# Performance work log

Hardware: AMD Instinct MI355X
Metric: run time of the kernel (lower is better)

Reference implementation:

```python
import jax, jax.numpy as jnp
import numpy as np

N, T, ENC_H, ATT_H, DEC_H, OUT, SPK = 32, 4096, 512, 256, 512, 80, 64
ATT_RANGE = 10
KW = 31  # conv kernel width, padding 15


def softsign(x):
    return x / (1.0 + jnp.abs(x))


def setup_inputs() -> dict:
    key = jax.random.key(0)
    ks = jax.random.split(key, 20)
    lengths_enc = jax.random.randint(ks[0], (N,), 2048, T + 1)
    pos = jnp.arange(T)
    prev_attention = jax.random.uniform(ks[1], (N, T, 1), jnp.float32)
    # zero attention beyond valid length (so argmax lies within length, as in practice)
    prev_attention = prev_attention * (pos[None, :, None] < lengths_enc[:, None, None])
    s = 0.05
    inp = {
        "input_enc": jax.random.normal(ks[2], (N, T, ENC_H), jnp.float32),
        "input_dec": jax.random.normal(ks[3], (N, 1, OUT), jnp.float32),
        "prev_attention": prev_attention,
        "spkr_vec": jax.random.normal(ks[4], (N, 1, SPK), jnp.float32),
        "lengths_enc": lengths_enc,
        "speed": jax.random.uniform(ks[5], (N,), jnp.float32),
        # parameters (torch Linear: y = x @ W.T + b; we store W already transposed)
        "W_enc": jax.random.normal(ks[6], (ENC_H, ATT_H), jnp.float32) * s,
        "b_enc": jnp.zeros((ATT_H,), jnp.float32),
        "W_spkr": jax.random.normal(ks[7], (SPK, ATT_H), jnp.float32) * s,
        "conv_w": jax.random.normal(ks[8], (ATT_H, 1, KW), jnp.float32) * s,  # OIH
        "W_dec": jax.random.normal(ks[9], (DEC_H, ATT_H), jnp.float32) * s,
        "W_speed": jax.random.normal(ks[10], (1, ATT_H), jnp.float32) * s,
        "Wp1": jax.random.normal(ks[11], (OUT + SPK, 2 * DEC_H), jnp.float32) * s,
        "bp1": jnp.zeros((2 * DEC_H,), jnp.float32),
        "Wp2": jax.random.normal(ks[12], (2 * DEC_H, DEC_H), jnp.float32) * s,
        "bp2": jnp.zeros((DEC_H,), jnp.float32),
        "W_proj": jax.random.normal(ks[13], (ATT_H, 1), jnp.float32) * s,
        "b_proj": jnp.zeros((1,), jnp.float32),
    }
    return inp


def reference(input_enc, input_dec, prev_attention, spkr_vec, lengths_enc, speed,
              W_enc, b_enc, W_spkr, conv_w, W_dec, W_speed,
              Wp1, bp1, Wp2, bp2, W_proj, b_proj):
    # prenet (dropout = identity in eval mode)
    dec_in = jnp.concatenate([input_dec, spkr_vec], axis=-1)          # [N,1,OUT+SPK]
    h = jax.nn.relu(dec_in @ Wp1 + bp1)                               # [N,1,2*DEC_H]
    out_prenet = jax.nn.relu(h @ Wp2 + bp2)                           # [N,1,DEC_H]

    # biases (computed fresh, null_bias branch)
    att_bias_speed = (speed[:, None] @ W_speed)[:, None, :]           # [N,1,ATT_H]
    att_bias_enc = softsign(input_enc @ W_enc + b_enc)                # [N,T,ATT_H]
    att_bias_spkr = softsign(spkr_vec @ W_spkr)                       # [N,1,ATT_H]

    # location conv: [N,T,1] -> [N,1,T] -> conv(k=31,p=15) -> [N,ATT_H,T] -> [N,T,ATT_H]
    conv = jax.lax.conv_general_dilated(
        prev_attention.transpose(0, 2, 1), conv_w,
        window_strides=(1,), padding=[(15, 15)],
        dimension_numbers=("NCH", "OIH", "NCH"))
    in_att_prev_att = conv.transpose(0, 2, 1)                         # [N,T,ATT_H]

    in_att_dec = out_prenet @ W_dec                                   # [N,1,ATT_H]

    e = att_bias_enc + in_att_dec + att_bias_spkr + in_att_prev_att + att_bias_speed
    logit = jnp.tanh(e) @ W_proj + b_proj                             # [N,T,1]

    # windowed band mask around argmax of prev attention (no_grad in torch)
    max_idx = jnp.argmax(prev_attention[:, :, 0], axis=1)             # [N]
    lo = jnp.maximum(max_idx - (ATT_RANGE - 1), 0)
    hi = jnp.minimum(max_idx + (ATT_RANGE - 1), lengths_enc - 1)
    pos = jnp.arange(T)
    att_mask = ((pos[None, :] >= lo[:, None]) & (pos[None, :] <= hi[:, None]))
    att_mask = att_mask[:, :, None].astype(logit.dtype)               # [N,T,1]

    logit_max = jnp.max(logit, axis=1, keepdims=True)
    curr = jnp.exp(logit - logit_max) * att_mask
    denom = jnp.maximum(jnp.sum(jnp.abs(curr), axis=1, keepdims=True), 1e-12)
    return curr / denom
```

## Files before the change

### kernel.cpp

```cpp
#include <hip/hip_runtime.h>
#include <hip/hip_bf16.h>

#define NB     32
#define TLEN   4096
#define ENCH   512
#define ATTH   256
#define OUTD   80
#define SPKD   64
#define KW     31
#define ATTR   10

__global__ __launch_bounds__(1024) void fused_kernel(
    const float* __restrict__ input_enc,
    const float* __restrict__ input_dec,
    const float* __restrict__ pa,
    const float* __restrict__ spkr_vec,
    const int*   __restrict__ lengths,
    const float* __restrict__ speed,
    const float* __restrict__ W_enc,
    const float* __restrict__ b_enc,
    const float* __restrict__ W_spkr,
    const float* __restrict__ conv_w,
    const float* __restrict__ W_dec,
    const float* __restrict__ W_speed,
    const float* __restrict__ Wp1,
    const float* __restrict__ bp1,
    const float* __restrict__ Wp2,
    const float* __restrict__ bp2,
    const float* __restrict__ W_proj,
    float* __restrict__ out)
{
  const int n   = blockIdx.x;
  const int tid = threadIdx.x;

  __shared__ float s_dec[144];
  __shared__ float s_h1[1024];
  __shared__ float s_op[512];
  __shared__ __align__(16) float s_red[8 * 512];
  __shared__ float s_av[1024];
  __shared__ int   s_ai[1024];
  __shared__ float s_bias[256];
  __shared__ float s_enc[4][ENCH];
  __shared__ float s_pa[52];
  __shared__ float s_part[16];
  __shared__ float s_logits[20];
  __shared__ int   s_lo, s_hi;

  ((float4*)(out + (size_t)n * TLEN))[tid] = make_float4(0.f, 0.f, 0.f, 0.f);

  if (tid < OUTD)      s_dec[tid] = input_dec[n * OUTD + tid];
  else if (tid < 144)  s_dec[tid] = spkr_vec[n * SPKD + (tid - OUTD)];

  {
    const float* p = pa + (size_t)n * TLEN;
    float bv = -1.f; int bi = 0;
    #pragma unroll
    for (int k = 0; k < TLEN / 1024; k++) {
      int t = tid + k * 1024;
      float v = p[t];
      if (v > bv) { bv = v; bi = t; }
    }
    s_av[tid] = bv; s_ai[tid] = bi;
    __syncthreads();
    for (int s = 512; s > 0; s >>= 1) {
      if (tid < s) {
        float ov = s_av[tid + s]; int oi = s_ai[tid + s];
        float mv = s_av[tid];     int mi = s_ai[tid];
        if (ov > mv || (ov == mv && oi < mi)) { s_av[tid] = ov; s_ai[tid] = oi; }
      }
      __syncthreads();
    }
    if (tid == 0) {
      int mi = s_ai[0];
      s_lo = max(mi - (ATTR - 1), 0);
      s_hi = min(mi + (ATTR - 1), lengths[n] - 1);
    }
  }

  {
    float acc = bp1[tid];
    #pragma unroll 4
    for (int i = 0; i < 144; i++)
      acc = fmaf(s_dec[i], Wp1[i * 1024 + tid], acc);
    s_h1[tid] = fmaxf(acc, 0.f);
  }
  __syncthreads();

  if (tid < 52) {
    int idx = s_lo - (KW / 2) + tid;
    s_pa[tid] = (idx >= 0 && idx < TLEN) ? pa[(size_t)n * TLEN + idx] : 0.f;
  }

  {
    const int g = tid & 127, sl = tid >> 7;
    const int k0 = g * 4;
    float4 acc = make_float4(0.f, 0.f, 0.f, 0.f);
    for (int j = sl; j < 1024; j += 8) {
      float hv = s_h1[j];
      float4 w = *(const float4*)(Wp2 + (size_t)j * 512 + k0);
      acc.x = fmaf(hv, w.x, acc.x);
      acc.y = fmaf(hv, w.y, acc.y);
      acc.z = fmaf(hv, w.z, acc.z);
      acc.w = fmaf(hv, w.w, acc.w);
    }
    *(float4*)(s_red + sl * 512 + k0) = acc;
    __syncthreads();
    if (tid < 512) {
      float v = bp2[tid];
      #pragma unroll
      for (int s2 = 0; s2 < 8; s2++) v += s_red[s2 * 512 + tid];
      s_op[tid] = fmaxf(v, 0.f);
    }
    __syncthreads();
  }

  {
    const int c = tid & 255, sl = tid >> 8;
    float acc = 0.f;
    const int kb = sl * 128;
    #pragma unroll 4
    for (int k = kb; k < kb + 128; k++)
      acc = fmaf(s_op[k], W_dec[k * 256 + c], acc);
    s_red[sl * 256 + c] = acc;
    __syncthreads();
    if (tid < 256) {
      float b = s_red[tid] + s_red[256 + tid] + s_red[512 + tid] + s_red[768 + tid];
      float sp = 0.f;
      #pragma unroll 4
      for (int i = 0; i < 64; i++)
        sp = fmaf(s_dec[OUTD + i], W_spkr[i * 256 + tid], sp);
      sp = sp / (1.f + fabsf(sp));
      s_bias[tid] = b + sp + speed[n] * W_speed[tid];
    }
  }
  __syncthreads();

  const int lo = s_lo, hi = s_hi;
  const int q  = tid >> 8;
  const int c  = tid & 255;
  const float be = b_enc[c];
  const float wp = W_proj[c];
  const float bs = s_bias[c];

  for (int g = 0; g < 5; g++) {
    {
      int e0 = tid, e1 = tid + 1024;
      int q0 = e0 >> 9, i0 = e0 & 511;
      int q1 = e1 >> 9, i1 = e1 & 511;
      int t0 = lo + g * 4 + q0;
      int t1 = lo + g * 4 + q1;
      s_enc[q0][i0] = (t0 <= hi) ? input_enc[((size_t)n * TLEN + t0) * ENCH + i0] : 0.f;
      s_enc[q1][i1] = (t1 <= hi) ? input_enc[((size_t)n * TLEN + t1) * ENCH + i1] : 0.f;
    }
    __syncthreads();

    float a0 = 0.f, a1 = 0.f;
    #pragma unroll 8
    for (int i = 0; i < ENCH; i += 2) {
      a0 = fmaf(s_enc[q][i],     W_enc[i * 256 + c],       a0);
      a1 = fmaf(s_enc[q][i + 1], W_enc[(i + 1) * 256 + c], a1);
    }
    float a = a0 + a1;

    const int slot = g * 4 + q;
    float cv = 0.f;
    #pragma unroll
    for (int k = 0; k < KW; k++)
      cv = fmaf(s_pa[slot + k], conv_w[c * KW + k], cv);

    float ss = a + be;
    ss = ss / (1.f + fabsf(ss));
    float v = tanhf(ss + bs + cv) * wp;

    #pragma unroll
    for (int off = 32; off > 0; off >>= 1) v += __shfl_down(v, off);
    if ((tid & 63) == 0) s_part[tid >> 6] = v;
    __syncthreads();
    if (tid < 4) {
      float s = s_part[tid * 4] + s_part[tid * 4 + 1]
              + s_part[tid * 4 + 2] + s_part[tid * 4 + 3];
      int t = lo + g * 4 + tid;
      s_logits[g * 4 + tid] = (t <= hi) ? s : -__builtin_inff();
    }
    __syncthreads();
  }

  if (tid < 64) {
    float l = (tid < 20) ? s_logits[tid] : -__builtin_inff();
    float m = l;
    #pragma unroll
    for (int off = 32; off > 0; off >>= 1) m = fmaxf(m, __shfl_down(m, off));
    m = __shfl(m, 0);
    float e = __expf(l - m);
    float s = e;
    #pragma unroll
    for (int off = 32; off > 0; off >>= 1) s += __shfl_down(s, off);
    s = __shfl(s, 0);
    int t = lo + tid;
    if (tid < 20 && t <= hi)
      out[(size_t)n * TLEN + t] = e / s;
  }
}

extern "C" void kernel_launch(void* const* d_in, const int* in_sizes, int n_in,
                              void* d_out, int out_size, void* d_ws, size_t ws_size,
                              hipStream_t stream) {
  const float* input_enc = (const float*)d_in[0];
  const float* input_dec = (const float*)d_in[1];
  const float* pa        = (const float*)d_in[2];
  const float* spkr_vec  = (const float*)d_in[3];
  const int*   lengths   = (const int*)  d_in[4];
  const float* speed     = (const float*)d_in[5];
  const float* W_enc     = (const float*)d_in[6];
  const float* b_enc     = (const float*)d_in[7];
  const float* W_spkr    = (const float*)d_in[8];
  const float* conv_w    = (const float*)d_in[9];
  const float* W_dec     = (const float*)d_in[10];
  const float* W_speed   = (const float*)d_in[11];
  const float* Wp1       = (const float*)d_in[12];
  const float* bp1       = (const float*)d_in[13];
  const float* Wp2       = (const float*)d_in[14];
  const float* bp2       = (const float*)d_in[15];
  const float* W_proj    = (const float*)d_in[16];

  float* out = (float*)d_out;

  hipLaunchKernelGGL(fused_kernel, dim3(NB), dim3(1024), 0, stream,
                     input_enc, input_dec, pa, spkr_vec, lengths, speed,
                     W_enc, b_enc, W_spkr, conv_w, W_dec, W_speed,
                     Wp1, bp1, Wp2, bp2, W_proj, out);
}
```

Before: 507.5 us.

## Split fused kernel into prep, per-timestep band, and softmax kernels

Splits the single 32-block fused kernel into three launches. A prep kernel computes the argmax window and the per-batch bias into workspace. A band kernel runs a 32x20 grid, one block per windowed timestep, with a float4-vectorized W_enc GEMV and conv weights staged in shared memory. A small softmax kernel finishes the normalization. This spreads the serial band loop across many more CUs, at the cost of two extra launches and workspace round-trips.

```diff
diff --git a/kernel.cpp b/kernel.cpp
--- a/kernel.cpp
+++ b/kernel.cpp
@@ -10,25 +10,22 @@
 #define KW     31
 #define ATTR   10
 
-__global__ __launch_bounds__(1024) void fused_kernel(
-    const float* __restrict__ input_enc,
+__global__ __launch_bounds__(1024) void prep_kernel(
+    const float* __restrict__ pa,
     const float* __restrict__ input_dec,
-    const float* __restrict__ pa,
     const float* __restrict__ spkr_vec,
-    const int*   __restrict__ lengths,
     const float* __restrict__ speed,
-    const float* __restrict__ W_enc,
-    const float* __restrict__ b_enc,
-    const float* __restrict__ W_spkr,
-    const float* __restrict__ conv_w,
-    const float* __restrict__ W_dec,
-    const float* __restrict__ W_speed,
     const float* __restrict__ Wp1,
     const float* __restrict__ bp1,
     const float* __restrict__ Wp2,
     const float* __restrict__ bp2,
-    const float* __restrict__ W_proj,
-    float* __restrict__ out)
+    const float* __restrict__ W_dec,
+    const float* __restrict__ W_spkr,
+    const float* __restrict__ W_speed,
+    const int*   __restrict__ lengths,
+    float* __restrict__ out,
+    int* __restrict__ ws_idx,
+    float* __restrict__ ws_bias)
 {
   const int n   = blockIdx.x;
   const int tid = threadIdx.x;
@@ -39,12 +36,6 @@
   __shared__ __align__(16) float s_red[8 * 512];
   __shared__ float s_av[1024];
   __shared__ int   s_ai[1024];
-  __shared__ float s_bias[256];
-  __shared__ float s_enc[4][ENCH];
-  __shared__ float s_pa[52];
-  __shared__ float s_part[16];
-  __shared__ float s_logits[20];
-  __shared__ int   s_lo, s_hi;
 
   ((float4*)(out + (size_t)n * TLEN))[tid] = make_float4(0.f, 0.f, 0.f, 0.f);
 
@@ -72,8 +63,8 @@
     }
     if (tid == 0) {
       int mi = s_ai[0];
-      s_lo = max(mi - (ATTR - 1), 0);
-      s_hi = min(mi + (ATTR - 1), lengths[n] - 1);
+      ws_idx[n * 2]     = max(mi - (ATTR - 1), 0);
+      ws_idx[n * 2 + 1] = min(mi + (ATTR - 1), lengths[n] - 1);
     }
   }
 
@@ -85,11 +76,6 @@
     s_h1[tid] = fmaxf(acc, 0.f);
   }
   __syncthreads();
-
-  if (tid < 52) {
-    int idx = s_lo - (KW / 2) + tid;
-    s_pa[tid] = (idx >= 0 && idx < TLEN) ? pa[(size_t)n * TLEN + idx] : 0.f;
-  }
 
   {
     const int g = tid & 127, sl = tid >> 7;
@@ -130,76 +116,113 @@
       for (int i = 0; i < 64; i++)
         sp = fmaf(s_dec[OUTD + i], W_spkr[i * 256 + tid], sp);
       sp = sp / (1.f + fabsf(sp));
-      s_bias[tid] = b + sp + speed[n] * W_speed[tid];
-    }
-  }
-  __syncthreads();
-
-  const int lo = s_lo, hi = s_hi;
-  const int q  = tid >> 8;
-  const int c  = tid & 255;
-  const float be = b_enc[c];
-  const float wp = W_proj[c];
-  const float bs = s_bias[c];
-
-  for (int g = 0; g < 5; g++) {
-    {
-      int e0 = tid, e1 = tid + 1024;
-      int q0 = e0 >> 9, i0 = e0 & 511;
-      int q1 = e1 >> 9, i1 = e1 & 511;
-      int t0 = lo + g * 4 + q0;
-      int t1 = lo + g * 4 + q1;
-      s_enc[q0][i0] = (t0 <= hi) ? input_enc[((size_t)n * TLEN + t0) * ENCH + i0] : 0.f;
-      s_enc[q1][i1] = (t1 <= hi) ? input_enc[((size_t)n * TLEN + t1) * ENCH + i1] : 0.f;
-    }
-    __syncthreads();
-
-    float a0 = 0.f, a1 = 0.f;
+      ws_bias[n * 256 + tid] = b + sp + speed[n] * W_speed[tid];
+    }
+  }
+}
+
+__global__ __launch_bounds__(256) void band_kernel(
+    const float* __restrict__ input_enc,
+    const float* __restrict__ pa,
+    const float* __restrict__ W_enc,
+    const float* __restrict__ b_enc,
+    const float* __restrict__ conv_w,
+    const float* __restrict__ W_proj,
+    const int*   __restrict__ ws_idx,
+    const float* __restrict__ ws_bias,
+    float* __restrict__ ws_logits)
+{
+  const int n   = blockIdx.x;
+  const int j   = blockIdx.y;
+  const int tid = threadIdx.x;
+
+  const int lo = ws_idx[n * 2];
+  const int hi = ws_idx[n * 2 + 1];
+  const int t  = lo + j;
+
+  if (t > hi) {
+    if (tid == 0) ws_logits[n * 20 + j] = -__builtin_inff();
+    return;
+  }
+
+  __shared__ __align__(16) float s_enc[ENCH];
+  __shared__ float s_pa[KW];
+  __shared__ __align__(16) float s_red[4 * 256];
+  __shared__ float s_cw[ATTH * KW];
+  __shared__ float s_part[4];
+
+  for (int k2 = tid; k2 < ATTH * KW; k2 += 256) s_cw[k2] = conv_w[k2];
+  if (tid < 128)
+    ((float4*)s_enc)[tid] = ((const float4*)(input_enc + ((size_t)n * TLEN + t) * ENCH))[tid];
+  else if (tid < 128 + KW) {
+    int idx = t - (KW / 2) + (tid - 128);
+    s_pa[tid - 128] = (idx >= 0 && idx < TLEN) ? pa[(size_t)n * TLEN + idx] : 0.f;
+  }
+  __syncthreads();
+
+  {
+    const int sl = tid >> 6;
+    const int l4 = tid & 63;
+    const float4* W4 = (const float4*)W_enc;
+    float4 acc = make_float4(0.f, 0.f, 0.f, 0.f);
+    const int i0 = sl * 128;
     #pragma unroll 8
-    for (int i = 0; i < ENCH; i += 2) {
-      a0 = fmaf(s_enc[q][i],     W_enc[i * 256 + c],       a0);
-      a1 = fmaf(s_enc[q][i + 1], W_enc[(i + 1) * 256 + c], a1);
-    }
-    float a = a0 + a1;
-
-    const int slot = g * 4 + q;
+    for (int i = i0; i < i0 + 128; i++) {
+      float e  = s_enc[i];
+      float4 w = W4[i * 64 + l4];
+      acc.x = fmaf(e, w.x, acc.x);
+      acc.y = fmaf(e, w.y, acc.y);
+      acc.z = fmaf(e, w.z, acc.z);
+      acc.w = fmaf(e, w.w, acc.w);
+    }
+    *(float4*)(s_red + sl * 256 + l4 * 4) = acc;
+  }
+  __syncthreads();
+
+  {
+    const int c = tid;
+    float y = s_red[c] + s_red[256 + c] + s_red[512 + c] + s_red[768 + c];
     float cv = 0.f;
     #pragma unroll
     for (int k = 0; k < KW; k++)
-      cv = fmaf(s_pa[slot + k], conv_w[c * KW + k], cv);
-
-    float ss = a + be;
+      cv = fmaf(s_pa[k], s_cw[c * KW + k], cv);
+    float ss = y + b_enc[c];
     ss = ss / (1.f + fabsf(ss));
-    float v = tanhf(ss + bs + cv) * wp;
+    float v = tanhf(ss + ws_bias[n * 256 + c] + cv) * W_proj[c];
 
     #pragma unroll
     for (int off = 32; off > 0; off >>= 1) v += __shfl_down(v, off);
     if ((tid & 63) == 0) s_part[tid >> 6] = v;
-    __syncthreads();
-    if (tid < 4) {
-      float s = s_part[tid * 4] + s_part[tid * 4 + 1]
-              + s_part[tid * 4 + 2] + s_part[tid * 4 + 3];
-      int t = lo + g * 4 + tid;
-      s_logits[g * 4 + tid] = (t <= hi) ? s : -__builtin_inff();
-    }
-    __syncthreads();
-  }
-
-  if (tid < 64) {
-    float l = (tid < 20) ? s_logits[tid] : -__builtin_inff();
-    float m = l;
-    #pragma unroll
-    for (int off = 32; off > 0; off >>= 1) m = fmaxf(m, __shfl_down(m, off));
-    m = __shfl(m, 0);
-    float e = __expf(l - m);
-    float s = e;
-    #pragma unroll
-    for (int off = 32; off > 0; off >>= 1) s += __shfl_down(s, off);
-    s = __shfl(s, 0);
-    int t = lo + tid;
-    if (tid < 20 && t <= hi)
-      out[(size_t)n * TLEN + t] = e / s;
-  }
+  }
+  __syncthreads();
+  if (tid == 0)
+    ws_logits[n * 20 + j] = s_part[0] + s_part[1] + s_part[2] + s_part[3];
+}
+
+__global__ __launch_bounds__(64) void softmax_kernel(
+    const float* __restrict__ ws_logits,
+    const int*   __restrict__ ws_idx,
+    float* __restrict__ out)
+{
+  const int n   = blockIdx.x;
+  const int tid = threadIdx.x;
+  const int lo  = ws_idx[n * 2];
+  const int hi  = ws_idx[n * 2 + 1];
+
+  float l = (tid < 20) ? ws_logits[n * 20 + tid] : -__builtin_inff();
+  float m = l;
+  #pragma unroll
+  for (int off = 32; off > 0; off >>= 1) m = fmaxf(m, __shfl_down(m, off));
+  m = __shfl(m, 0);
+  float e = __expf(l - m);
+  float s = e;
+  #pragma unroll
+  for (int off = 32; off > 0; off >>= 1) s += __shfl_down(s, off);
+  s = __shfl(s, 0);
+
+  int t = lo + tid;
+  if (tid < 20 && t <= hi)
+    out[(size_t)n * TLEN + t] = e / s;
 }
 
 extern "C" void kernel_launch(void* const* d_in, const int* in_sizes, int n_in,
@@ -225,8 +248,18 @@
 
   float* out = (float*)d_out;
 
-  hipLaunchKernelGGL(fused_kernel, dim3(NB), dim3(1024), 0, stream,
-                     input_enc, input_dec, pa, spkr_vec, lengths, speed,
-                     W_enc, b_enc, W_spkr, conv_w, W_dec, W_speed,
-                     Wp1, bp1, Wp2, bp2, W_proj, out);
-}
+  int*   ws_idx    = (int*)d_ws;
+  float* ws_bias   = (float*)((char*)d_ws + 256);
+  float* ws_logits = (float*)((char*)d_ws + 256 + NB * 256 * 4);
+
+  hipLaunchKernelGGL(prep_kernel, dim3(NB), dim3(1024), 0, stream,
+                     pa, input_dec, spkr_vec, speed, Wp1, bp1, Wp2, bp2,
+                     W_dec, W_spkr, W_speed, lengths, out, ws_idx, ws_bias);
+
+  hipLaunchKernelGGL(band_kernel, dim3(NB, 20), dim3(256), 0, stream,
+                     input_enc, pa, W_enc, b_enc, conv_w, W_proj,
+                     ws_idx, ws_bias, ws_logits);
+
+  hipLaunchKernelGGL(softmax_kernel, dim3(NB), dim3(64), 0, stream,
+                     ws_logits, ws_idx, out);
+}
```

New measurement: 441.1 us. -13.1%, faster.
